# Optimization experiments

Hardware: AMD Instinct MI355X
Metric: run time of the kernel (lower is better)

Reference implementation:

```python
import jax, jax.numpy as jnp
import numpy as np

N_TOKENS = 32768
LATENT_DIM = 512
N_EMBED = 8192
BETA_COMMIT = 0.25


def setup_inputs() -> dict:
    key = jax.random.key(0)
    k_x, k_w, _ = jax.random.split(key, 3)
    x = jax.random.normal(k_x, (N_TOKENS, LATENT_DIM), dtype=jnp.float32)
    # nn.init.uniform_ -> U[0, 1)
    W = jax.random.uniform(k_w, (N_EMBED, LATENT_DIM), dtype=jnp.float32)
    temperature = jnp.ones((1,), dtype=jnp.float32)
    return {"x": x, "temperature": temperature, "W": W}


def reference(x, temperature, W):
    # out_proj is Identity (sim_vq=False, codebook_normalization=False)
    codebook = W  # [K, D]
    # Squared-Euclidean pairwise distances: [N, K]
    dist = (
        jnp.sum(x * x, axis=1, keepdims=True)
        + jnp.sum(codebook * codebook, axis=1)[None, :]
        - 2.0 * (x @ codebook.T)
    )
    ids = jnp.argmin(dist, axis=1)  # [N]
    emb = codebook[ids]             # gather nearest code, [N, D]
    # Straight-through estimator (training STE path)
    emb_out = x + jax.lax.stop_gradient(emb - x)
    # QuantizeLoss(beta): codebook loss + beta * commitment loss
    codebook_loss = jnp.mean(jnp.sum((jax.lax.stop_gradient(x) - emb) ** 2, axis=-1))
    commit_loss = jnp.mean(jnp.sum((x - jax.lax.stop_gradient(emb)) ** 2, axis=-1))
    loss = codebook_loss + BETA_COMMIT * commit_loss
    return emb_out, ids, loss
```

## Files before the change

### kernel.cpp

```cpp
#include <hip/hip_runtime.h>
#include <math.h>

#define NTOK 32768
#define DIM 512
#define KC 8192

#define TBM 128
#define TBN 128
#define HSTEPS 16
#define PSTEP 4096

typedef unsigned short u16;
typedef _Float16 half8 __attribute__((ext_vector_type(8)));
typedef float f32x4 __attribute__((ext_vector_type(4)));

__device__ __forceinline__ void gload16(const void* g, void* l) {
    __builtin_amdgcn_global_load_lds(
        (const __attribute__((address_space(1))) unsigned int*)(void*)g,
        (__attribute__((address_space(3))) unsigned int*)l, 16, 0, 0);
}

__global__ __launch_bounds__(256) void c2_kernel(const float* __restrict__ W,
                                                 float* __restrict__ c2) {
    int wid = threadIdx.x >> 6;
    int lane = threadIdx.x & 63;
    int row = blockIdx.x * 4 + wid;
    const float* wr = W + (size_t)row * DIM;
    float s = 0.f;
#pragma unroll
    for (int q = 0; q < 2; ++q) {
        float4 v = *(const float4*)(wr + q * 256 + lane * 4);
        s += v.x * v.x + v.y * v.y + v.z * v.z + v.w * v.w;
    }
#pragma unroll
    for (int off = 32; off > 0; off >>= 1) s += __shfl_down(s, off);
    if (lane == 0) c2[row] = s;
}

__global__ __launch_bounds__(256) void loss_kernel(const float* __restrict__ partials,
                                                   float* __restrict__ lossp) {
    __shared__ float red[256];
    float s = 0.f;
    for (int idx = threadIdx.x; idx < NTOK / 4; idx += 256) s += partials[idx];
    red[threadIdx.x] = s;
    __syncthreads();
    for (int off = 128; off > 0; off >>= 1) {
        if (threadIdx.x < off) red[threadIdx.x] += red[threadIdx.x + off];
        __syncthreads();
    }
    if (threadIdx.x == 0) lossp[0] = 1.25f * red[0] / (float)NTOK;
}

__global__ void init_keys_kernel(unsigned long long* keys) {
    keys[blockIdx.x * 256 + threadIdx.x] = ~0ull;
}

__global__ __launch_bounds__(256) void split_kernel(const float* __restrict__ src,
                                                    u16* __restrict__ dst) {
    int lane = threadIdx.x & 63;
    int wid = threadIdx.x >> 6;
    int row = blockIdx.x * 64 + lane;
    int s = blockIdx.y * 4 + wid;
    const float* p = src + (size_t)row * DIM + s * 32;
    int tile = row >> 7, Rl = row & 127, swz = (Rl >> 1) & 3;
    u16* baseH = dst + ((size_t)(tile * 32 + s) * 128 + Rl) * 32;
    u16* baseL = baseH + (size_t)16 * PSTEP;
#pragma unroll
    for (int c = 0; c < 4; ++c) {
        float4 va = ((const float4*)p)[c * 2];
        float4 vb = ((const float4*)p)[c * 2 + 1];
        float f[8] = {va.x, va.y, va.z, va.w, vb.x, vb.y, vb.z, vb.w};
        unsigned H[4], L[4];
#pragma unroll
        for (int j = 0; j < 4; ++j) {
            _Float16 h0 = (_Float16)f[2 * j];
            _Float16 g0 = (_Float16)(f[2 * j] - (float)h0);
            _Float16 h1 = (_Float16)f[2 * j + 1];
            _Float16 g1 = (_Float16)(f[2 * j + 1] - (float)h1);
            H[j] = (unsigned)__builtin_bit_cast(u16, h0) |
                   ((unsigned)__builtin_bit_cast(u16, h1) << 16);
            L[j] = (unsigned)__builtin_bit_cast(u16, g0) |
                   ((unsigned)__builtin_bit_cast(u16, g1) << 16);
        }
        int slot = (c ^ swz) * 8;
        *(uint4*)(baseH + slot) = uint4{H[0], H[1], H[2], H[3]};
        *(uint4*)(baseL + slot) = uint4{L[0], L[1], L[2], L[3]};
    }
}

__global__ __launch_bounds__(256, 2) void argmin_mfma_kernel(
    const u16* __restrict__ xscr, const u16* __restrict__ wscr,
    const float* __restrict__ c2, unsigned long long* __restrict__ keys) {
    __shared__ __align__(16) u16 AH[2][PSTEP];
    __shared__ __align__(16) u16 AL[2][PSTEP];
    __shared__ __align__(16) u16 BH[2][PSTEP];
    __shared__ __align__(16) u16 BL[2][PSTEP];

    int cpx = (int)gridDim.x >> 3;
    int bid = (int)blockIdx.x;
    int wg = (bid & 7) * cpx + (bid >> 3);
    int tcol = wg & 63;
    int trow = wg >> 6;

    const int tid = threadIdx.x;
    const int lane = tid & 63;
    const int w = tid >> 6;
    const int wr = w >> 1;
    const int wc = w & 1;

    const u16* gA = xscr + (size_t)trow * (32 * PSTEP);
    const u16* gB = wscr + (size_t)tcol * (32 * PSTEP);

    const int l15 = lane & 15, q = lane >> 4;
    float c2v[4];
    const int colbase = tcol * 128 + wc * 64 + l15;
#pragma unroll
    for (int n = 0; n < 4; ++n) c2v[n] = c2[colbase + n * 16];

    f32x4 acc[4][4];
#pragma unroll
    for (int m = 0; m < 4; ++m)
#pragma unroll
        for (int n = 0; n < 4; ++n) acc[m][n] = f32x4{0.f, 0.f, 0.f, 0.f};

    const int swz = (l15 >> 1) & 3;
    const int soff = (q ^ swz) * 8;
    const int arow = (wr * 64 + l15) * 32;
    const int brow = (wc * 64 + l15) * 32;
    const int wo = w * 1024;
    const int lo8 = lane * 8;

    {
        const u16* ah = gA;                       const u16* al = gA + 16 * PSTEP;
        const u16* bh = gB;                       const u16* bl = gB + 16 * PSTEP;
        gload16(ah + wo + lo8, AH[0] + wo);       gload16(ah + wo + 512 + lo8, AH[0] + wo + 512);
        gload16(al + wo + lo8, AL[0] + wo);       gload16(al + wo + 512 + lo8, AL[0] + wo + 512);
        gload16(bh + wo + lo8, BH[0] + wo);       gload16(bh + wo + 512 + lo8, BH[0] + wo + 512);
        gload16(bl + wo + lo8, BL[0] + wo);       gload16(bl + wo + 512 + lo8, BL[0] + wo + 512);
    }

#pragma unroll 2
    for (int c = 0; c < HSTEPS; ++c) {
        const int b = c & 1;
        asm volatile("s_waitcnt vmcnt(0)" ::: "memory");
        __builtin_amdgcn_s_barrier();
        __builtin_amdgcn_sched_barrier(0);

        if (c + 1 < HSTEPS) {
            const u16* ah = gA + (size_t)(c + 1) * PSTEP;
            const u16* al = ah + 16 * PSTEP;
            const u16* bh = gB + (size_t)(c + 1) * PSTEP;
            const u16* bl = bh + 16 * PSTEP;
            u16* dah = AH[b ^ 1]; u16* dal = AL[b ^ 1];
            u16* dbh = BH[b ^ 1]; u16* dbl = BL[b ^ 1];
            gload16(ah + wo + lo8, dah + wo);     gload16(ah + wo + 512 + lo8, dah + wo + 512);
            gload16(al + wo + lo8, dal + wo);     gload16(al + wo + 512 + lo8, dal + wo + 512);
            gload16(bh + wo + lo8, dbh + wo);     gload16(bh + wo + 512 + lo8, dbh + wo + 512);
            gload16(bl + wo + lo8, dbl + wo);     gload16(bl + wo + 512 + lo8, dbl + wo + 512);
        }

        half8 bhv[4], ahv[4];
#pragma unroll
        for (int n = 0; n < 4; ++n) bhv[n] = *(const half8*)(BH[b] + brow + n * 512 + soff);
#pragma unroll
        for (int m = 0; m < 4; ++m) ahv[m] = *(const half8*)(AH[b] + arow + m * 512 + soff);
        __builtin_amdgcn_s_setprio(1);
#pragma unroll
        for (int m = 0; m < 4; ++m)
#pragma unroll
            for (int n = 0; n < 4; ++n)
                acc[m][n] = __builtin_amdgcn_mfma_f32_16x16x32_f16(ahv[m], bhv[n], acc[m][n], 0, 0, 0);
        __builtin_amdgcn_s_setprio(0);

        half8 alv[4];
#pragma unroll
        for (int m = 0; m < 4; ++m) alv[m] = *(const half8*)(AL[b] + arow + m * 512 + soff);
        __builtin_amdgcn_s_setprio(1);
#pragma unroll
        for (int m = 0; m < 4; ++m)
#pragma unroll
            for (int n = 0; n < 4; ++n)
                acc[m][n] = __builtin_amdgcn_mfma_f32_16x16x32_f16(alv[m], bhv[n], acc[m][n], 0, 0, 0);
        __builtin_amdgcn_s_setprio(0);

        half8 blv[4];
#pragma unroll
        for (int n = 0; n < 4; ++n) blv[n] = *(const half8*)(BL[b] + brow + n * 512 + soff);
        __builtin_amdgcn_s_setprio(1);
#pragma unroll
        for (int m = 0; m < 4; ++m)
#pragma unroll
            for (int n = 0; n < 4; ++n)
                acc[m][n] = __builtin_amdgcn_mfma_f32_16x16x32_f16(ahv[m], blv[n], acc[m][n], 0, 0, 0);
        __builtin_amdgcn_s_setprio(0);
    }

    unsigned long long* kbuf = (unsigned long long*)&AH[0][0];
#pragma unroll
    for (int m = 0; m < 4; ++m) {
#pragma unroll
        for (int r = 0; r < 4; ++r) {
            float bv = 3.4e38f;
            int bi = 0;
#pragma unroll
            for (int n = 0; n < 4; ++n) {
                float sc = c2v[n] - 2.0f * acc[m][n][r];
                int idx = colbase + n * 16;
                if (sc < bv) { bv = sc; bi = idx; }
            }
#pragma unroll
            for (int off = 1; off < 16; off <<= 1) {
                float ov = __shfl_xor(bv, off);
                int oi = __shfl_xor(bi, off);
                if (ov < bv || (ov == bv && oi < bi)) { bv = ov; bi = oi; }
            }
            if (l15 == 0) {
                unsigned u = __float_as_uint(bv);
                u = (u & 0x80000000u) ? ~u : (u | 0x80000000u);
                kbuf[wc * 128 + wr * 64 + m * 16 + q * 4 + r] =
                    ((unsigned long long)u << 32) | (unsigned)bi;
            }
        }
    }
    __syncthreads();
    if (tid < 128) {
        unsigned long long k = kbuf[tid];
        unsigned long long o = kbuf[128 + tid];
        if (o < k) k = o;
        atomicMin(&keys[trow * 128 + tid], k);
    }
}

__global__ __launch_bounds__(256) void gather_keys_kernel(
    const float* __restrict__ x, const float* __restrict__ W,
    const unsigned long long* __restrict__ keys, float* __restrict__ emb_out,
    float* __restrict__ idsf, float* __restrict__ partials) {
    int wid = threadIdx.x >> 6;
    int lane = threadIdx.x & 63;
    int tok = blockIdx.x * 4 + wid;
    int id = (int)(unsigned)(keys[tok] & 0xffffffffull);
    if (lane == 0) idsf[tok] = (float)id;
    const float* wr = W + (size_t)id * DIM;
    const float* xr = x + (size_t)tok * DIM;
    float* orow = emb_out + (size_t)tok * DIM;
    float s = 0.f;
#pragma unroll
    for (int q = 0; q < 2; ++q) {
        int d = q * 256 + lane * 4;
        float4 wv = *(const float4*)(wr + d);
        float4 xv = *(const float4*)(xr + d);
        float4 e = {xv.x + (wv.x - xv.x), xv.y + (wv.y - xv.y),
                    xv.z + (wv.z - xv.z), xv.w + (wv.w - xv.w)};
        *(float4*)(orow + d) = e;
        float dx = xv.x - wv.x, dy = xv.y - wv.y, dz = xv.z - wv.z, dw = xv.w - wv.w;
        s += dx * dx + dy * dy + dz * dz + dw * dw;
    }
#pragma unroll
    for (int off = 32; off > 0; off >>= 1) s += __shfl_down(s, off);
    __shared__ float bsum[4];
    if (lane == 0) bsum[wid] = s;
    __syncthreads();
    if (threadIdx.x == 0)
        partials[blockIdx.x] = bsum[0] + bsum[1] + bsum[2] + bsum[3];
}

#define FBN 64
#define FBK 64
#define FDC 32
#define FPAD 68
__global__ __launch_bounds__(256) void argmin_kernel(const float* __restrict__ x,
                                                     const float* __restrict__ W,
                                                     const float* __restrict__ c2,
                                                     float* __restrict__ idsf) {
    __shared__ float xs[FDC][FPAD];
    __shared__ float wt[FDC][FPAD];
    __shared__ float c2s[FBK];
    __shared__ float redv[16][FBN];
    __shared__ int redi[16][FBN];
    const int tid = threadIdx.x;
    const int n0 = blockIdx.x * FBN;
    const int i = tid & 15;
    const int j = tid >> 4;
    float bestv[4];
    int besti[4];
#pragma unroll
    for (int t = 0; t < 4; ++t) { bestv[t] = 3.4e38f; besti[t] = 0; }
    for (int k0 = 0; k0 < KC; k0 += FBK) {
        __syncthreads();
        if (tid < FBK) c2s[tid] = c2[k0 + tid];
        float acc[4][4];
#pragma unroll
        for (int a = 0; a < 4; ++a)
#pragma unroll
            for (int b = 0; b < 4; ++b) acc[a][b] = 0.f;
        for (int d0 = 0; d0 < DIM; d0 += FDC) {
            __syncthreads();
#pragma unroll
            for (int r = 0; r < 2; ++r) {
                int f = tid + r * 256;
                int tok = f >> 3;
                int dq = f & 7;
                float4 xv = *(const float4*)(x + (size_t)(n0 + tok) * DIM + d0 + dq * 4);
                float4 wv = *(const float4*)(W + (size_t)(k0 + tok) * DIM + d0 + dq * 4);
                xs[dq * 4 + 0][tok] = xv.x; xs[dq * 4 + 1][tok] = xv.y;
                xs[dq * 4 + 2][tok] = xv.z; xs[dq * 4 + 3][tok] = xv.w;
                wt[dq * 4 + 0][tok] = wv.x; wt[dq * 4 + 1][tok] = wv.y;
                wt[dq * 4 + 2][tok] = wv.z; wt[dq * 4 + 3][tok] = wv.w;
            }
            __syncthreads();
#pragma unroll
            for (int d = 0; d < FDC; ++d) {
                float4 xv = *(const float4*)(&xs[d][i * 4]);
                float4 wv = *(const float4*)(&wt[d][j * 4]);
#pragma unroll
                for (int a = 0; a < 4; ++a) {
                    float xa = (a == 0) ? xv.x : (a == 1) ? xv.y : (a == 2) ? xv.z : xv.w;
                    acc[a][0] = fmaf(xa, wv.x, acc[a][0]);
                    acc[a][1] = fmaf(xa, wv.y, acc[a][1]);
                    acc[a][2] = fmaf(xa, wv.z, acc[a][2]);
                    acc[a][3] = fmaf(xa, wv.w, acc[a][3]);
                }
            }
        }
#pragma unroll
        for (int ti = 0; ti < 4; ++ti)
#pragma unroll
            for (int cj = 0; cj < 4; ++cj) {
                float s = c2s[j * 4 + cj] - 2.f * acc[ti][cj];
                int kk = k0 + j * 4 + cj;
                if (s < bestv[ti]) { bestv[ti] = s; besti[ti] = kk; }
            }
    }
#pragma unroll
    for (int ti = 0; ti < 4; ++ti) {
        redv[j][i * 4 + ti] = bestv[ti];
        redi[j][i * 4 + ti] = besti[ti];
    }
    __syncthreads();
    if (tid < FBN) {
        float bv = redv[0][tid];
        int bi = redi[0][tid];
#pragma unroll
        for (int jj = 1; jj < 16; ++jj) {
            float v = redv[jj][tid];
            int ii = redi[jj][tid];
            if (v < bv || (v == bv && ii < bi)) { bv = v; bi = ii; }
        }
        idsf[n0 + tid] = (float)bi;
    }
}

__global__ __launch_bounds__(256) void gather_kernel(const float* __restrict__ x,
                                                     const float* __restrict__ W,
                                                     const float* __restrict__ idsf,
                                                     float* __restrict__ emb_out,
                                                     float* __restrict__ partials) {
    int wid = threadIdx.x >> 6;
    int lane = threadIdx.x & 63;
    int tok = blockIdx.x * 4 + wid;
    int id = (int)idsf[tok];
    const float* wr = W + (size_t)id * DIM;
    const float* xr = x + (size_t)tok * DIM;
    float* orow = emb_out + (size_t)tok * DIM;
    float s = 0.f;
#pragma unroll
    for (int q = 0; q < 2; ++q) {
        int d = q * 256 + lane * 4;
        float4 wv = *(const float4*)(wr + d);
        float4 xv = *(const float4*)(xr + d);
        float4 e = {xv.x + (wv.x - xv.x), xv.y + (wv.y - xv.y),
                    xv.z + (wv.z - xv.z), xv.w + (wv.w - xv.w)};
        *(float4*)(orow + d) = e;
        float dx = xv.x - wv.x, dy = xv.y - wv.y, dz = xv.z - wv.z, dw = xv.w - wv.w;
        s += dx * dx + dy * dy + dz * dz + dw * dw;
    }
#pragma unroll
    for (int off = 32; off > 0; off >>= 1) s += __shfl_down(s, off);
    __shared__ float bsum[4];
    if (lane == 0) bsum[wid] = s;
    __syncthreads();
    if (threadIdx.x == 0)
        partials[blockIdx.x] = bsum[0] + bsum[1] + bsum[2] + bsum[3];
}

extern "C" void kernel_launch(void* const* d_in, const int* in_sizes, int n_in,
                              void* d_out, int out_size, void* d_ws, size_t ws_size,
                              hipStream_t stream) {
    const float* x = (const float*)d_in[0];
    const float* W = (const float*)d_in[2];

    float* out = (float*)d_out;
    float* emb_out = out;
    float* idsf = out + (size_t)NTOK * DIM;
    float* lossp = idsf + NTOK;

    const size_t W12_BYTES = (size_t)KC * DIM * 4;
    const size_t KEYS_BYTES = (size_t)NTOK * 8;
    size_t need = W12_BYTES + KEYS_BYTES + (size_t)KC * 4 + (size_t)(NTOK / 4) * 4;

    if (ws_size >= need) {
        u16* w12 = (u16*)d_ws;
        unsigned long long* keys = (unsigned long long*)((char*)d_ws + W12_BYTES);
        float* c2 = (float*)((char*)keys + KEYS_BYTES);
        float* partials = c2 + KC;
        u16* x12 = (u16*)emb_out;

        split_kernel<<<dim3(NTOK / 64, 4), 256, 0, stream>>>(x, x12);
        split_kernel<<<dim3(KC / 64, 4), 256, 0, stream>>>(W, w12);
        c2_kernel<<<KC / 4, 256, 0, stream>>>(W, c2);
        init_keys_kernel<<<NTOK / 256, 256, 0, stream>>>(keys);
        argmin_mfma_kernel<<<(NTOK / TBM) * (KC / TBN), 256, 0, stream>>>(x12, w12, c2, keys);
        gather_keys_kernel<<<NTOK / 4, 256, 0, stream>>>(x, W, keys, emb_out, idsf, partials);
        loss_kernel<<<1, 256, 0, stream>>>(partials, lossp);
    } else {
        float* c2 = (float*)d_ws;
        float* partials = c2 + KC;
        c2_kernel<<<KC / 4, 256, 0, stream>>>(W, c2);
        argmin_kernel<<<NTOK / FBN, 256, 0, stream>>>(x, W, c2, idsf);
        gather_kernel<<<NTOK / 4, 256, 0, stream>>>(x, W, idsf, emb_out, partials);
        loss_kernel<<<1, 256, 0, stream>>>(partials, lossp);
    }
}
```

Baseline: 964.8 us.

## Load codebook fragments directly from global into registers, halve LDS footprint

The B (codebook) hi/lo tiles are no longer staged through shared memory. Each wave reads its MFMA fragments straight from global memory, using an unswizzled split layout for W. This halves LDS use per block, and the launch bound is raised to 3 blocks per CU to allow more occupancy. The risk is exposed global-load latency inside the main loop, since B loads are issued at the top of each step with no prefetch, plus redundant global reads of B across waves sharing a column tile.

```diff
diff --git a/kernel.cpp b/kernel.cpp
--- a/kernel.cpp
+++ b/kernel.cpp
@@ -55,6 +55,7 @@
     keys[blockIdx.x * 256 + threadIdx.x] = ~0ull;
 }
 
+template <int SWZ>
 __global__ __launch_bounds__(256) void split_kernel(const float* __restrict__ src,
                                                     u16* __restrict__ dst) {
     int lane = threadIdx.x & 63;
@@ -82,19 +83,17 @@
             L[j] = (unsigned)__builtin_bit_cast(u16, g0) |
                    ((unsigned)__builtin_bit_cast(u16, g1) << 16);
         }
-        int slot = (c ^ swz) * 8;
+        int slot = (SWZ ? (c ^ swz) : c) * 8;
         *(uint4*)(baseH + slot) = uint4{H[0], H[1], H[2], H[3]};
         *(uint4*)(baseL + slot) = uint4{L[0], L[1], L[2], L[3]};
     }
 }
 
-__global__ __launch_bounds__(256, 2) void argmin_mfma_kernel(
+__global__ __launch_bounds__(256, 3) void argmin_mfma_kernel(
     const u16* __restrict__ xscr, const u16* __restrict__ wscr,
     const float* __restrict__ c2, unsigned long long* __restrict__ keys) {
     __shared__ __align__(16) u16 AH[2][PSTEP];
     __shared__ __align__(16) u16 AL[2][PSTEP];
-    __shared__ __align__(16) u16 BH[2][PSTEP];
-    __shared__ __align__(16) u16 BL[2][PSTEP];
 
     int cpx = (int)gridDim.x >> 3;
     int bid = (int)blockIdx.x;
@@ -126,17 +125,17 @@
     const int swz = (l15 >> 1) & 3;
     const int soff = (q ^ swz) * 8;
     const int arow = (wr * 64 + l15) * 32;
-    const int brow = (wc * 64 + l15) * 32;
+    const int boff = (wc * 64 + l15) * 32 + q * 8;
     const int wo = w * 1024;
     const int lo8 = lane * 8;
 
     {
-        const u16* ah = gA;                       const u16* al = gA + 16 * PSTEP;
-        const u16* bh = gB;                       const u16* bl = gB + 16 * PSTEP;
-        gload16(ah + wo + lo8, AH[0] + wo);       gload16(ah + wo + 512 + lo8, AH[0] + wo + 512);
-        gload16(al + wo + lo8, AL[0] + wo);       gload16(al + wo + 512 + lo8, AL[0] + wo + 512);
-        gload16(bh + wo + lo8, BH[0] + wo);       gload16(bh + wo + 512 + lo8, BH[0] + wo + 512);
-        gload16(bl + wo + lo8, BL[0] + wo);       gload16(bl + wo + 512 + lo8, BL[0] + wo + 512);
+        const u16* ah = gA;
+        const u16* al = gA + 16 * PSTEP;
+        gload16(ah + wo + lo8, AH[0] + wo);
+        gload16(ah + wo + 512 + lo8, AH[0] + wo + 512);
+        gload16(al + wo + lo8, AL[0] + wo);
+        gload16(al + wo + 512 + lo8, AL[0] + wo + 512);
     }
 
 #pragma unroll 2
@@ -146,22 +145,27 @@
         __builtin_amdgcn_s_barrier();
         __builtin_amdgcn_sched_barrier(0);
 
+        const u16* bh = gB + (size_t)c * PSTEP;
+        const u16* bl = bh + 16 * PSTEP;
+        half8 bhv[4], blv[4];
+#pragma unroll
+        for (int n = 0; n < 4; ++n) {
+            bhv[n] = *(const half8*)(bh + boff + n * 512);
+            blv[n] = *(const half8*)(bl + boff + n * 512);
+        }
+
         if (c + 1 < HSTEPS) {
             const u16* ah = gA + (size_t)(c + 1) * PSTEP;
             const u16* al = ah + 16 * PSTEP;
-            const u16* bh = gB + (size_t)(c + 1) * PSTEP;
-            const u16* bl = bh + 16 * PSTEP;
-            u16* dah = AH[b ^ 1]; u16* dal = AL[b ^ 1];
-            u16* dbh = BH[b ^ 1]; u16* dbl = BL[b ^ 1];
-            gload16(ah + wo + lo8, dah + wo);     gload16(ah + wo + 512 + lo8, dah + wo + 512);
-            gload16(al + wo + lo8, dal + wo);     gload16(al + wo + 512 + lo8, dal + wo + 512);
-            gload16(bh + wo + lo8, dbh + wo);     gload16(bh + wo + 512 + lo8, dbh + wo + 512);
-            gload16(bl + wo + lo8, dbl + wo);     gload16(bl + wo + 512 + lo8, dbl + wo + 512);
-        }
-
-        half8 bhv[4], ahv[4];
-#pragma unroll
-        for (int n = 0; n < 4; ++n) bhv[n] = *(const half8*)(BH[b] + brow + n * 512 + soff);
+            u16* dah = AH[b ^ 1];
+            u16* dal = AL[b ^ 1];
+            gload16(ah + wo + lo8, dah + wo);
+            gload16(ah + wo + 512 + lo8, dah + wo + 512);
+            gload16(al + wo + lo8, dal + wo);
+            gload16(al + wo + 512 + lo8, dal + wo + 512);
+        }
+
+        half8 ahv[4];
 #pragma unroll
         for (int m = 0; m < 4; ++m) ahv[m] = *(const half8*)(AH[b] + arow + m * 512 + soff);
         __builtin_amdgcn_s_setprio(1);
@@ -181,12 +185,7 @@
 #pragma unroll
             for (int n = 0; n < 4; ++n)
                 acc[m][n] = __builtin_amdgcn_mfma_f32_16x16x32_f16(alv[m], bhv[n], acc[m][n], 0, 0, 0);
-        __builtin_amdgcn_s_setprio(0);
-
-        half8 blv[4];
-#pragma unroll
-        for (int n = 0; n < 4; ++n) blv[n] = *(const half8*)(BL[b] + brow + n * 512 + soff);
-        __builtin_amdgcn_s_setprio(1);
+
 #pragma unroll
         for (int m = 0; m < 4; ++m)
 #pragma unroll
@@ -405,8 +404,8 @@
         float* partials = c2 + KC;
         u16* x12 = (u16*)emb_out;
 
-        split_kernel<<<dim3(NTOK / 64, 4), 256, 0, stream>>>(x, x12);
-        split_kernel<<<dim3(KC / 64, 4), 256, 0, stream>>>(W, w12);
+        split_kernel<1><<<dim3(NTOK / 64, 4), 256, 0, stream>>>(x, x12);
+        split_kernel<0><<<dim3(KC / 64, 4), 256, 0, stream>>>(W, w12);
         c2_kernel<<<KC / 4, 256, 0, stream>>>(W, c2);
         init_keys_kernel<<<NTOK / 256, 256, 0, stream>>>(keys);
         argmin_mfma_kernel<<<(NTOK / TBM) * (KC / TBN), 256, 0, stream>>>(x12, w12, c2, keys);
```

After: 894.0 us, median of 2. 1.08x faster.
